# Performance work log

Hardware: AMD Instinct MI355X
Metric: run time of the kernel (lower is better)

Reference implementation:

```python
import jax, jax.numpy as jnp
import numpy as np
from jax.scipy.special import logsumexp

N, D, M = 131072, 32, 256


def setup_inputs() -> dict:
    key = jax.random.key(0)
    k1, k2, k3 = jax.random.split(key, 3)
    X = jax.random.normal(k1, (N, D), dtype=jnp.float32)
    center = jax.random.uniform(k2, (M, D), dtype=jnp.float32)
    # cov_inv_sqrt near identity so det(cov_inv) ~ 1 (fit() would init it via Cholesky);
    # random-matrix init would make det overflow/underflow.
    cov_inv_sqrt = (jnp.eye(D, dtype=jnp.float32)[None, :, :]
                    + 0.02 * jax.random.normal(k3, (M, D, D), dtype=jnp.float32))
    weight = jnp.ones((M,), dtype=jnp.float32)
    threshold = jnp.zeros((1,), dtype=jnp.float32)
    return {"X": X, "center": center, "cov_inv_sqrt": cov_inv_sqrt,
            "weight": weight, "threshold": threshold}


def reference(X, center, cov_inv_sqrt, weight, threshold):
    # refresh(): equal_clusters=True branch
    w = jnp.abs(weight)
    pr = w / w.sum()                                            # [M]
    cov_inv = jnp.einsum('mij,mkj->mik', cov_inv_sqrt, cov_inv_sqrt)  # L L^T, [M,D,D]
    coef = pr * jnp.sqrt(jnp.linalg.det(cov_inv))               # [M]

    # Mahalanobis: q_ij = (x_i - c_j)^T A_j (x_i - c_j), expanded to avoid [N,M,D]:
    #   q_ij = xx_i . A_j_flat - 2 x_i . (A_j c_j) + c_j^T A_j c_j
    n, d = X.shape
    m = center.shape[0]
    A_flat = cov_inv.reshape(m, d * d)                          # [M, D*D]
    xx = (X[:, :, None] * X[:, None, :]).reshape(n, d * d)      # [N, D*D]
    term1 = xx @ A_flat.T                                       # [N, M]
    Ac = jnp.einsum('mkl,ml->mk', cov_inv, center)              # [M, D]
    term2 = X @ Ac.T                                            # [N, M]
    term3 = jnp.einsum('mk,mk->m', center, Ac)                  # [M]
    d_ij = -0.5 * (term1 - 2.0 * term2 + term3[None, :])        # [N, M]

    # weighted logsumexp over clusters: log sum_j coef_j exp(d_ij)
    ll = logsumexp(d_ij, axis=1, b=coef[None, :])               # [N]
    return ll - threshold[0]
```

## Files before the change

kernel.cpp:

```cpp
#include <hip/hip_runtime.h>
#include <hip/hip_bf16.h>
#include <math.h>

#define NPTS 131072
#define DIM 32
#define MCL 256
#define NSTEP 18
#define BPTS 64
#define THREADS 256

typedef __attribute__((ext_vector_type(8))) short s8v;
typedef __attribute__((ext_vector_type(4))) short s4h;
typedef __attribute__((ext_vector_type(4))) float f32x4;

__device__ __forceinline__ unsigned short f2bf(float f) {
    union { float f; unsigned u; } v; v.f = f;
    unsigned r = v.u + 0x7fffu + ((v.u >> 16) & 1u);
    return (unsigned short)(r >> 16);
}

__global__ __launch_bounds__(256) void gmm_prep(
    const float* __restrict__ center,
    const float* __restrict__ L,
    const float* __restrict__ weight,
    short* __restrict__ G,
    float* __restrict__ cst)
{
    const int m = blockIdx.x;
    const int t = threadIdx.x;
    __shared__ float Ls[DIM][DIM + 1];
    __shared__ float As[DIM][DIM + 1];
    __shared__ float Acs[DIM];
    __shared__ float red[DIM];

    const float* Lm = L + m * DIM * DIM;
    for (int k = t; k < DIM * DIM; k += 256)
        Ls[k >> 5][k & 31] = Lm[k];
    __syncthreads();

    for (int idx = t; idx < DIM * DIM; idx += 256) {
        const int j = idx >> 5, l = idx & 31;
        float a = 0.f;
        #pragma unroll
        for (int d = 0; d < DIM; ++d) a = fmaf(Ls[j][d], Ls[l][d], a);
        As[j][l] = a;
    }
    __syncthreads();

    if (t < DIM) {
        float a = 0.f;
        #pragma unroll
        for (int l = 0; l < DIM; ++l) a = fmaf(As[t][l], center[m * DIM + l], a);
        Acs[t] = a;
        red[t] = a * center[m * DIM + t];
    }
    __syncthreads();

    const int mt = m >> 4, ml = m & 15;
    for (int idx = t; idx < NSTEP * 32; idx += 256) {
        const int s = idx >> 5, k = idx & 31;
        float c;
        if (s == 0)       c = As[k][k] - 1.0f;
        else if (s <= 15) c = 2.0f * As[k][(k + s) & 31];
        else if (s == 16) c = (k < 16) ? 2.0f * As[k][k + 16] : -2.0f * Acs[k - 16];
        else              c = (k < 16) ? -2.0f * Acs[k + 16] : 0.0f;
        G[s * 8192 + mt * 512 + (k >> 3) * 128 + ml * 8 + (k & 7)] = (short)f2bf(c);
    }

    if (t < 64) {
        float logdet = 0.f;
        if (t < DIM) {
            float col[DIM];
            #pragma unroll
            for (int r2 = 0; r2 < DIM; ++r2) col[r2] = Ls[r2][t];
            float prodabs = 1.0f;
            #pragma unroll
            for (int k = 0; k < DIM; ++k) {
                const float pv  = __shfl(col[k], k, 64);
                const float rpv = 1.0f / pv;
                const float cjk = col[k];
                #pragma unroll
                for (int t2 = k + 1; t2 < DIM; ++t2) {
                    const float f = __shfl(col[t2], k, 64) * rpv;
                    col[t2] = fmaf(-f, cjk, col[t2]);
                }
                prodabs *= fabsf(pv);
            }
            logdet = logf(prodabs);
        }

        float wsp = 0.f;
        for (int j = t; j < MCL; j += 64) wsp += fabsf(weight[j]);
        #pragma unroll
        for (int d2 = 1; d2 < 64; d2 <<= 1) wsp += __shfl_xor(wsp, d2, 64);

        if (t == 0) {
            float t3 = 0.f;
            #pragma unroll
            for (int j = 0; j < DIM; ++j) t3 += red[j];
            cst[m] = logf(fabsf(weight[m])) - logf(wsp) + logdet - 0.5f * t3;
        }
    }
}

template<int OFF2, int E>
__device__ __forceinline__ float welem(const s4h a0, const s4h a1, const s4h a2) {
    constexpr int idx = OFF2 + E;
    unsigned short h;
    if constexpr (idx < 4)      h = (unsigned short)a0[idx & 3];
    else if constexpr (idx < 8) h = (unsigned short)a1[idx & 3];
    else                        h = (unsigned short)a2[idx & 3];
    return __uint_as_float(((unsigned)h) << 16);
}

template<int S, int E>
__device__ __forceinline__ float xsel(const float (&xkr)[8], int kg) {
    if constexpr (S == 16)      return (kg < 2) ? xkr[E] : 1.0f;
    else if constexpr (S == 17) return (kg < 2) ? 1.0f : 0.0f;
    else                        return xkr[E];
}

template<int S, int Q, int OFF2>
__device__ __forceinline__ unsigned mkpair(const float (&xkr)[8], int kg,
                                           const s4h a0, const s4h a1, const s4h a2) {
    const float p0 = xsel<S, 2 * Q>(xkr, kg)     * welem<OFF2, 2 * Q>(a0, a1, a2);
    const float p1 = xsel<S, 2 * Q + 1>(xkr, kg) * welem<OFF2, 2 * Q + 1>(a0, a1, a2);
    __hip_bfloat162 h2 = __float22bfloat162_rn(make_float2(p0, p1));
    return *reinterpret_cast<unsigned*>(&h2);
}

template<int S>
__device__ __forceinline__ void k_step(
    const short* __restrict__ gw,
    const short* __restrict__ Xh,
    const int (&rowh)[2],
    const float (&xk)[2][8],
    s8v (&bf)[8],
    f32x4 (&acc)[2][8],
    int kg)
{
    constexpr int shv  = (S == 17) ? 16 : S;
    constexpr int off2 = shv & 3;
    const int bq = ((kg * 8 + shv) & 31) & ~3;

    s8v af[2];
    #pragma unroll
    for (int i = 0; i < 2; ++i) {
        const short* xr = Xh + rowh[i] + bq;
        const s4h a0 = *(const s4h*)(xr);
        const s4h a1 = *(const s4h*)(xr + 4);
        s4h a2 = a1;
        if constexpr (off2 != 0) a2 = *(const s4h*)(xr + 8);

        union { s8v v; unsigned u[4]; } U;
        U.u[0] = mkpair<S, 0, off2>(xk[i], kg, a0, a1, a2);
        U.u[1] = mkpair<S, 1, off2>(xk[i], kg, a0, a1, a2);
        U.u[2] = mkpair<S, 2, off2>(xk[i], kg, a0, a1, a2);
        U.u[3] = mkpair<S, 3, off2>(xk[i], kg, a0, a1, a2);
        af[i] = U.v;
    }

    #pragma unroll
    for (int i = 0; i < 2; ++i)
        #pragma unroll
        for (int j = 0; j < 8; ++j)
            acc[i][j] = __builtin_amdgcn_mfma_f32_16x16x32_bf16(
                af[i], bf[j], acc[i][j], 0, 0, 0);

    if constexpr (S + 1 < NSTEP) {
        #pragma unroll
        for (int j = 0; j < 8; ++j)
            bf[j] = *(const s8v*)(gw + (size_t)(S + 1) * 8192 + j * 512);
    }
    __builtin_amdgcn_sched_barrier(0);
}

template<int S>
__device__ __forceinline__ void k_loop(
    const short* __restrict__ gw, const short* __restrict__ Xh,
    const int (&rowh)[2], const float (&xk)[2][8],
    s8v (&bf)[8], f32x4 (&acc)[2][8], int kg)
{
    k_step<S>(gw, Xh, rowh, xk, bf, acc, kg);
    if constexpr (S + 1 < NSTEP)
        k_loop<S + 1>(gw, Xh, rowh, xk, bf, acc, kg);
}

__global__ __launch_bounds__(THREADS, 3) void gmm_mfma(
    const float* __restrict__ X,
    const short* __restrict__ G,
    const float* __restrict__ cstw,
    const float* __restrict__ thr,
    float* __restrict__ out)
{
    __shared__ __attribute__((aligned(16))) short Xh[BPTS * 44];
    __shared__ float nrm_s[BPTS];
    __shared__ float cst_s[MCL];
    __shared__ float lse_m[BPTS];
    __shared__ float lse_d[BPTS];

    const int tid  = threadIdx.x;
    const int lane = tid & 63;
    const int w    = tid >> 6;
    const int wr   = w & 1;
    const int wc   = w >> 1;
    const int r    = lane & 15;
    const int kg   = lane >> 4;
    const int P0   = blockIdx.x * BPTS;

    const short* gw = G + wc * 4096 + lane * 8;

    int rowh[2];
    float xk[2][8];
    #pragma unroll
    for (int i = 0; i < 2; ++i) {
        const int row = wr * 32 + i * 16 + r;
        rowh[i] = row * 44;
        const float4* xg = reinterpret_cast<const float4*>(
            X + (size_t)(P0 + row) * DIM + kg * 8);
        const float4 a = xg[0], b = xg[1];
        xk[i][0] = a.x; xk[i][1] = a.y; xk[i][2] = a.z; xk[i][3] = a.w;
        xk[i][4] = b.x; xk[i][5] = b.y; xk[i][6] = b.z; xk[i][7] = b.w;
    }

    {
        const int p = tid >> 1, hf = tid & 1;
        if (tid < 128) {
            const float4* Xg = reinterpret_cast<const float4*>(
                X + (size_t)(P0 + p) * DIM + hf * 16);
            float part = 0.f;
            #pragma unroll
            for (int q = 0; q < 4; ++q) {
                const float4 v = Xg[q];
                const int kb = hf * 16 + 4 * q;
                Xh[p * 44 + kb + 0] = (short)f2bf(v.x);
                Xh[p * 44 + kb + 1] = (short)f2bf(v.y);
                Xh[p * 44 + kb + 2] = (short)f2bf(v.z);
                Xh[p * 44 + kb + 3] = (short)f2bf(v.w);
                if (!hf && q < 2) {
                    Xh[p * 44 + 32 + kb + 0] = (short)f2bf(v.x);
                    Xh[p * 44 + 32 + kb + 1] = (short)f2bf(v.y);
                    Xh[p * 44 + 32 + kb + 2] = (short)f2bf(v.z);
                    Xh[p * 44 + 32 + kb + 3] = (short)f2bf(v.w);
                }
                part = fmaf(v.x, v.x, part); part = fmaf(v.y, v.y, part);
                part = fmaf(v.z, v.z, part); part = fmaf(v.w, v.w, part);
            }
            part += __shfl_xor(part, 1, 64);
            if (!hf) nrm_s[p] = part;
        }
        cst_s[tid] = cstw[tid];
    }

    s8v bf[8];
    #pragma unroll
    for (int j = 0; j < 8; ++j)
        bf[j] = *(const s8v*)(gw + j * 512);

    __syncthreads();

    f32x4 acc[2][8] = {};
    k_loop<0>(gw, Xh, rowh, xk, bf, acc, kg);

    float cstr[8];
    #pragma unroll
    for (int j = 0; j < 8; ++j)
        cstr[j] = cst_s[wc * 128 + j * 16 + r];

    float mx[8], sm[8];
    #pragma unroll
    for (int i = 0; i < 2; ++i)
        #pragma unroll
        for (int rg = 0; rg < 4; ++rg) {
            const int sl = i * 4 + rg;
            float m_ = -1e30f;
            #pragma unroll
            for (int j = 0; j < 8; ++j)
                m_ = fmaxf(m_, fmaf(acc[i][j][rg], -0.5f, cstr[j]));
            float s_ = 0.f;
            #pragma unroll
            for (int j = 0; j < 8; ++j)
                s_ += __expf(fmaf(acc[i][j][rg], -0.5f, cstr[j]) - m_);
            mx[sl] = m_; sm[sl] = s_;
        }

    #pragma unroll
    for (int d = 1; d < 16; d <<= 1) {
        #pragma unroll
        for (int sl = 0; sl < 8; ++sl) {
            const float pm = __shfl_xor(mx[sl], d, 64);
            const float ps = __shfl_xor(sm[sl], d, 64);
            const float nm = fmaxf(mx[sl], pm);
            sm[sl] = sm[sl] * __expf(mx[sl] - nm) + ps * __expf(pm - nm);
            mx[sl] = nm;
        }
    }

    if (wc == 0 && r == 0) {
        #pragma unroll
        for (int i = 0; i < 2; ++i)
            #pragma unroll
            for (int rg = 0; rg < 4; ++rg) {
                const int p2 = wr * 32 + i * 16 + kg * 4 + rg;
                lse_m[p2] = mx[i * 4 + rg];
                lse_d[p2] = sm[i * 4 + rg];
            }
    }
    __syncthreads();
    if (wc == 1 && r == 0) {
        const float thrv = thr[0];
        #pragma unroll
        for (int i = 0; i < 2; ++i)
            #pragma unroll
            for (int rg = 0; rg < 4; ++rg) {
                const int sl = i * 4 + rg;
                const int p2 = wr * 32 + i * 16 + kg * 4 + rg;
                const float om = lse_m[p2], os = lse_d[p2];
                const float nm = fmaxf(mx[sl], om);
                const float ss = sm[sl] * __expf(mx[sl] - nm) + os * __expf(om - nm);
                out[P0 + p2] = nm + __logf(ss) - 0.5f * nrm_s[p2] - thrv;
            }
    }
}

extern "C" void kernel_launch(void* const* d_in, const int* in_sizes, int n_in,
                              void* d_out, int out_size, void* d_ws, size_t ws_size,
                              hipStream_t stream)
{
    const float* X      = (const float*)d_in[0];
    const float* center = (const float*)d_in[1];
    const float* L      = (const float*)d_in[2];
    const float* weight = (const float*)d_in[3];
    const float* thr    = (const float*)d_in[4];
    float* out = (float*)d_out;

    float* cst = (float*)d_ws;
    short* G   = (short*)((char*)d_ws + 1024);

    gmm_prep<<<MCL, 256, 0, stream>>>(center, L, weight, G, cst);
    gmm_mfma<<<NPTS / BPTS, THREADS, 0, stream>>>(X, G, cst, thr, out);
}
```

Before: 75.02 us.

## Switch MFMA operand path from bf16 to fp16 with packed half multiplies

Stores the quadratic-form coefficients and the X tile as fp16 instead of bf16 and uses the f16 MFMA. Operand products are now formed with packed half2 multiplies and alignbit word extraction, replacing per-element fp32 multiply plus bf16 repack. The S=0 diagonal step no longer reads LDS. The logsumexp reduction now takes the max across lanes before summing exponentials, which removes the pairwise rescaling exps. The fp16 range is narrower than bf16, so products of large x values or coefficients could overflow or lose accuracy.

```diff
diff --git a/kernel.cpp b/kernel.cpp
--- a/kernel.cpp
+++ b/kernel.cpp
@@ -9,14 +9,14 @@
 #define BPTS 64
 #define THREADS 256
 
-typedef __attribute__((ext_vector_type(8))) short s8v;
-typedef __attribute__((ext_vector_type(4))) short s4h;
+typedef __attribute__((ext_vector_type(8))) _Float16 f16x8;
+typedef __attribute__((ext_vector_type(2))) _Float16 h2v;
+typedef __attribute__((ext_vector_type(2))) unsigned u2v;
 typedef __attribute__((ext_vector_type(4))) float f32x4;
 
-__device__ __forceinline__ unsigned short f2bf(float f) {
-    union { float f; unsigned u; } v; v.f = f;
-    unsigned r = v.u + 0x7fffu + ((v.u >> 16) & 1u);
-    return (unsigned short)(r >> 16);
+__device__ __forceinline__ short f2h(float f) {
+    _Float16 h = (_Float16)f;
+    union { _Float16 h; short s; } X; X.h = h; return X.s;
 }
 
 __global__ __launch_bounds__(256) void gmm_prep(
@@ -64,7 +64,7 @@
         else if (s <= 15) c = 2.0f * As[k][(k + s) & 31];
         else if (s == 16) c = (k < 16) ? 2.0f * As[k][k + 16] : -2.0f * Acs[k - 16];
         else              c = (k < 16) ? -2.0f * Acs[k + 16] : 0.0f;
-        G[s * 8192 + mt * 512 + (k >> 3) * 128 + ml * 8 + (k & 7)] = (short)f2bf(c);
+        G[s * 8192 + mt * 512 + (k >> 3) * 128 + ml * 8 + (k & 7)] = f2h(c);
     }
 
     if (t < 64) {
@@ -103,30 +103,42 @@
     }
 }
 
-template<int OFF2, int E>
-__device__ __forceinline__ float welem(const s4h a0, const s4h a1, const s4h a2) {
-    constexpr int idx = OFF2 + E;
-    unsigned short h;
-    if constexpr (idx < 4)      h = (unsigned short)a0[idx & 3];
-    else if constexpr (idx < 8) h = (unsigned short)a1[idx & 3];
-    else                        h = (unsigned short)a2[idx & 3];
-    return __uint_as_float(((unsigned)h) << 16);
-}
-
-template<int S, int E>
-__device__ __forceinline__ float xsel(const float (&xkr)[8], int kg) {
-    if constexpr (S == 16)      return (kg < 2) ? xkr[E] : 1.0f;
-    else if constexpr (S == 17) return (kg < 2) ? 1.0f : 0.0f;
-    else                        return xkr[E];
+template<int J>
+__device__ __forceinline__ unsigned wword(const u2v b0, const u2v b1, const u2v b2) {
+    if constexpr (J < 2)      return b0[J];
+    else if constexpr (J < 4) return b1[J - 2];
+    else                      return b2[J - 4];
+}
+
+template<int OFF2, int Q>
+__device__ __forceinline__ h2v wpair(const u2v b0, const u2v b1, const u2v b2) {
+    constexpr int idx0 = OFF2 + 2 * Q;
+    constexpr int wj = idx0 >> 1;
+    unsigned u;
+    if constexpr ((idx0 & 1) == 0)
+        u = wword<wj>(b0, b1, b2);
+    else
+        u = __builtin_amdgcn_alignbit(wword<wj + 1>(b0, b1, b2),
+                                      wword<wj>(b0, b1, b2), 16);
+    union { unsigned u; h2v h; } X; X.u = u; return X.h;
 }
 
 template<int S, int Q, int OFF2>
-__device__ __forceinline__ unsigned mkpair(const float (&xkr)[8], int kg,
-                                           const s4h a0, const s4h a1, const s4h a2) {
-    const float p0 = xsel<S, 2 * Q>(xkr, kg)     * welem<OFF2, 2 * Q>(a0, a1, a2);
-    const float p1 = xsel<S, 2 * Q + 1>(xkr, kg) * welem<OFF2, 2 * Q + 1>(a0, a1, a2);
-    __hip_bfloat162 h2 = __float22bfloat162_rn(make_float2(p0, p1));
-    return *reinterpret_cast<unsigned*>(&h2);
+__device__ __forceinline__ h2v mkpair(const h2v (&xp)[4], int kg,
+                                      const u2v b0, const u2v b1, const u2v b2) {
+    if constexpr (S == 0) {
+        return xp[Q] * xp[Q];
+    } else {
+        const h2v wp = wpair<OFF2, Q>(b0, b1, b2);
+        if constexpr (S == 16) {
+            return (kg < 2) ? (h2v)(xp[Q] * wp) : wp;
+        } else if constexpr (S == 17) {
+            const h2v z = { (_Float16)0.f, (_Float16)0.f };
+            return (kg < 2) ? wp : z;
+        } else {
+            return xp[Q] * wp;
+        }
+    }
 }
 
 template<int S>
@@ -134,8 +146,8 @@
     const short* __restrict__ gw,
     const short* __restrict__ Xh,
     const int (&rowh)[2],
-    const float (&xk)[2][8],
-    s8v (&bf)[8],
+    const h2v (&xp)[2][4],
+    f16x8 (&bf)[8],
     f32x4 (&acc)[2][8],
     int kg)
 {
@@ -143,20 +155,21 @@
     constexpr int off2 = shv & 3;
     const int bq = ((kg * 8 + shv) & 31) & ~3;
 
-    s8v af[2];
+    f16x8 af[2];
     #pragma unroll
     for (int i = 0; i < 2; ++i) {
-        const short* xr = Xh + rowh[i] + bq;
-        const s4h a0 = *(const s4h*)(xr);
-        const s4h a1 = *(const s4h*)(xr + 4);
-        s4h a2 = a1;
-        if constexpr (off2 != 0) a2 = *(const s4h*)(xr + 8);
-
-        union { s8v v; unsigned u[4]; } U;
-        U.u[0] = mkpair<S, 0, off2>(xk[i], kg, a0, a1, a2);
-        U.u[1] = mkpair<S, 1, off2>(xk[i], kg, a0, a1, a2);
-        U.u[2] = mkpair<S, 2, off2>(xk[i], kg, a0, a1, a2);
-        U.u[3] = mkpair<S, 3, off2>(xk[i], kg, a0, a1, a2);
+        u2v b0 = {}, b1 = {}, b2 = {};
+        if constexpr (S != 0) {
+            const short* xr = Xh + rowh[i] + bq;
+            b0 = *(const u2v*)(xr);
+            b1 = *(const u2v*)(xr + 4);
+            if constexpr (off2 != 0) b2 = *(const u2v*)(xr + 8);
+        }
+        union { f16x8 v; h2v p[4]; } U;
+        U.p[0] = mkpair<S, 0, off2>(xp[i], kg, b0, b1, b2);
+        U.p[1] = mkpair<S, 1, off2>(xp[i], kg, b0, b1, b2);
+        U.p[2] = mkpair<S, 2, off2>(xp[i], kg, b0, b1, b2);
+        U.p[3] = mkpair<S, 3, off2>(xp[i], kg, b0, b1, b2);
         af[i] = U.v;
     }
 
@@ -164,13 +177,13 @@
     for (int i = 0; i < 2; ++i)
         #pragma unroll
         for (int j = 0; j < 8; ++j)
-            acc[i][j] = __builtin_amdgcn_mfma_f32_16x16x32_bf16(
+            acc[i][j] = __builtin_amdgcn_mfma_f32_16x16x32_f16(
                 af[i], bf[j], acc[i][j], 0, 0, 0);
 
     if constexpr (S + 1 < NSTEP) {
         #pragma unroll
         for (int j = 0; j < 8; ++j)
-            bf[j] = *(const s8v*)(gw + (size_t)(S + 1) * 8192 + j * 512);
+            bf[j] = *(const f16x8*)(gw + (size_t)(S + 1) * 8192 + j * 512);
     }
     __builtin_amdgcn_sched_barrier(0);
 }
@@ -178,12 +191,12 @@
 template<int S>
 __device__ __forceinline__ void k_loop(
     const short* __restrict__ gw, const short* __restrict__ Xh,
-    const int (&rowh)[2], const float (&xk)[2][8],
-    s8v (&bf)[8], f32x4 (&acc)[2][8], int kg)
-{
-    k_step<S>(gw, Xh, rowh, xk, bf, acc, kg);
+    const int (&rowh)[2], const h2v (&xp)[2][4],
+    f16x8 (&bf)[8], f32x4 (&acc)[2][8], int kg)
+{
+    k_step<S>(gw, Xh, rowh, xp, bf, acc, kg);
     if constexpr (S + 1 < NSTEP)
-        k_loop<S + 1>(gw, Xh, rowh, xk, bf, acc, kg);
+        k_loop<S + 1>(gw, Xh, rowh, xp, bf, acc, kg);
 }
 
 __global__ __launch_bounds__(THREADS, 3) void gmm_mfma(
@@ -211,7 +224,7 @@
     const short* gw = G + wc * 4096 + lane * 8;
 
     int rowh[2];
-    float xk[2][8];
+    h2v xp[2][4];
     #pragma unroll
     for (int i = 0; i < 2; ++i) {
         const int row = wr * 32 + i * 16 + r;
@@ -219,8 +232,10 @@
         const float4* xg = reinterpret_cast<const float4*>(
             X + (size_t)(P0 + row) * DIM + kg * 8);
         const float4 a = xg[0], b = xg[1];
-        xk[i][0] = a.x; xk[i][1] = a.y; xk[i][2] = a.z; xk[i][3] = a.w;
-        xk[i][4] = b.x; xk[i][5] = b.y; xk[i][6] = b.z; xk[i][7] = b.w;
+        xp[i][0] = h2v{ (_Float16)a.x, (_Float16)a.y };
+        xp[i][1] = h2v{ (_Float16)a.z, (_Float16)a.w };
+        xp[i][2] = h2v{ (_Float16)b.x, (_Float16)b.y };
+        xp[i][3] = h2v{ (_Float16)b.z, (_Float16)b.w };
     }
 
     {
@@ -233,15 +248,15 @@
             for (int q = 0; q < 4; ++q) {
                 const float4 v = Xg[q];
                 const int kb = hf * 16 + 4 * q;
-                Xh[p * 44 + kb + 0] = (short)f2bf(v.x);
-                Xh[p * 44 + kb + 1] = (short)f2bf(v.y);
-                Xh[p * 44 + kb + 2] = (short)f2bf(v.z);
-                Xh[p * 44 + kb + 3] = (short)f2bf(v.w);
+                Xh[p * 44 + kb + 0] = f2h(v.x);
+                Xh[p * 44 + kb + 1] = f2h(v.y);
+                Xh[p * 44 + kb + 2] = f2h(v.z);
+                Xh[p * 44 + kb + 3] = f2h(v.w);
                 if (!hf && q < 2) {
-                    Xh[p * 44 + 32 + kb + 0] = (short)f2bf(v.x);
-                    Xh[p * 44 + 32 + kb + 1] = (short)f2bf(v.y);
-                    Xh[p * 44 + 32 + kb + 2] = (short)f2bf(v.z);
-                    Xh[p * 44 + 32 + kb + 3] = (short)f2bf(v.w);
+                    Xh[p * 44 + 32 + kb + 0] = f2h(v.x);
+                    Xh[p * 44 + 32 + kb + 1] = f2h(v.y);
+                    Xh[p * 44 + 32 + kb + 2] = f2h(v.z);
+                    Xh[p * 44 + 32 + kb + 3] = f2h(v.w);
                 }
                 part = fmaf(v.x, v.x, part); part = fmaf(v.y, v.y, part);
                 part = fmaf(v.z, v.z, part); part = fmaf(v.w, v.w, part);
@@ -252,15 +267,15 @@
         cst_s[tid] = cstw[tid];
     }
 
-    s8v bf[8];
+    f16x8 bf[8];
     #pragma unroll
     for (int j = 0; j < 8; ++j)
-        bf[j] = *(const s8v*)(gw + j * 512);
+        bf[j] = *(const f16x8*)(gw + j * 512);
 
     __syncthreads();
 
     f32x4 acc[2][8] = {};
-    k_loop<0>(gw, Xh, rowh, xk, bf, acc, kg);
+    k_loop<0>(gw, Xh, rowh, xp, bf, acc, kg);
 
     float cstr[8];
     #pragma unroll
@@ -277,24 +292,18 @@
             #pragma unroll
             for (int j = 0; j < 8; ++j)
                 m_ = fmaxf(m_, fmaf(acc[i][j][rg], -0.5f, cstr[j]));
+            #pragma unroll
+            for (int d = 1; d < 16; d <<= 1)
+                m_ = fmaxf(m_, __shfl_xor(m_, d, 64));
             float s_ = 0.f;
             #pragma unroll
             for (int j = 0; j < 8; ++j)
                 s_ += __expf(fmaf(acc[i][j][rg], -0.5f, cstr[j]) - m_);
+            #pragma unroll
+            for (int d = 1; d < 16; d <<= 1)
+                s_ += __shfl_xor(s_, d, 64);
             mx[sl] = m_; sm[sl] = s_;
         }
-
-    #pragma unroll
-    for (int d = 1; d < 16; d <<= 1) {
-        #pragma unroll
-        for (int sl = 0; sl < 8; ++sl) {
-            const float pm = __shfl_xor(mx[sl], d, 64);
-            const float ps = __shfl_xor(sm[sl], d, 64);
-            const float nm = fmaxf(mx[sl], pm);
-            sm[sl] = sm[sl] * __expf(mx[sl] - nm) + ps * __expf(pm - nm);
-            mx[sl] = nm;
-        }
-    }
 
     if (wc == 0 && r == 0) {
         #pragma unroll
```

Measured after the change: 68.80 us. 8.3% less time.
